# Kernel optimization log

Hardware: AMD Instinct MI355X
Metric: run time of the kernel (lower is better)

The kernel has to match this reference:

```python
import jax, jax.numpy as jnp
import numpy as np

N_EMBD = 768

def setup_inputs() -> dict:
    key = jax.random.key(0)
    k1, k2, k3, k4 = jax.random.split(key, 4)
    B, T, head_size = 16, 1024, 128
    x = jax.random.normal(k1, (B, T, N_EMBD), dtype=jnp.float32)
    # nn.Linear(in, out, bias=False): weight stored as (out, in); we store transposed (in, out)
    s = 1.0 / np.sqrt(N_EMBD)
    Wk = jax.random.uniform(k2, (N_EMBD, head_size), jnp.float32, -s, s)
    Wq = jax.random.uniform(k3, (N_EMBD, head_size), jnp.float32, -s, s)
    Wv = jax.random.uniform(k4, (N_EMBD, head_size), jnp.float32, -s, s)
    return {"x": x, "Wk": Wk, "Wq": Wq, "Wv": Wv}

def reference(x, Wk, Wq, Wv):
    B, T, C = x.shape  # C == n_embd == 768
    k = jnp.einsum('btc,ch->bth', x, Wk)
    q = jnp.einsum('btc,ch->bth', x, Wq)
    v = jnp.einsum('btc,ch->bth', x, Wv)
    # NOTE: original scales by C**-0.5 with C = n_embd (768), not head_size.
    wei = jnp.einsum('bth,bsh->bts', q, k) * (C ** -0.5)  # (B, T, T)
    causal = jnp.tril(jnp.ones((T, T), dtype=bool))
    wei = jnp.where(causal, wei, -jnp.inf)
    wei = jax.nn.softmax(wei, axis=-1)
    # dropout p=0.0 -> identity
    return jnp.einsum('bts,bsh->bth', wei, v)
```

## Files before the change

### kernel.cpp

```cpp
#include <hip/hip_runtime.h>
#include <math.h>

#define NTOK   16384
#define NEMBD  768
#define HDIM   128

typedef __attribute__((ext_vector_type(8)))  short short8;
typedef __attribute__((ext_vector_type(16))) float floatx16;

#define MFMA32(a,b,c) __builtin_amdgcn_mfma_f32_32x32x16_bf16(a,b,c,0,0,0)

__device__ __forceinline__ unsigned short f2bf(float f) {
    unsigned u = __float_as_uint(f);
    u += 0x7fff + ((u >> 16) & 1);
    return (unsigned short)(u >> 16);
}
__device__ __forceinline__ unsigned pack2(float a, float b) {
    return (unsigned)f2bf(a) | ((unsigned)f2bf(b) << 16);
}
__device__ __forceinline__ unsigned pack2_trunc(float a, float b) {
    return __builtin_amdgcn_perm(__float_as_uint(b), __float_as_uint(a),
                                 0x07060302u);
}
__device__ __forceinline__ void gl_lds16(const void* gptr, void* lptr) {
    __builtin_amdgcn_global_load_lds(
        (const __attribute__((address_space(1))) unsigned int*)gptr,
        (__attribute__((address_space(3))) unsigned int*)lptr, 16, 0, 0);
}

__global__ __launch_bounds__(256) void prep_w(
    const float* __restrict__ Wk, const float* __restrict__ Wq,
    const float* __restrict__ Wv, unsigned short* __restrict__ wt)
{
    __shared__ float T[64 * 65];

    const int tid = threadIdx.x;
    const int bw  = blockIdx.x / 24;
    const int rem = blockIdx.x % 24;
    const int ct  = rem >> 1, dh = rem & 1;
    const int c0  = ct * 64, d0 = dh * 64;
    const float* W = (bw == 0) ? Wk : ((bw == 1) ? Wq : Wv);
    const float scale = (bw == 1)
        ? (0.03608439182435161f * 1.4426950408889634f) : 1.0f;

    #pragma unroll
    for (int pass = 0; pass < 4; ++pass) {
        int idx = pass * 256 + tid;
        int c  = idx >> 4;
        int d4 = idx & 15;
        float4 v = ((const float4*)W)[(size_t)(c0 + c) * 32 + dh * 16 + d4];
        v.x *= scale; v.y *= scale; v.z *= scale; v.w *= scale;
        T[(d4 * 4 + 0) * 65 + c] = v.x;
        T[(d4 * 4 + 1) * 65 + c] = v.y;
        T[(d4 * 4 + 2) * 65 + c] = v.z;
        T[(d4 * 4 + 3) * 65 + c] = v.w;
    }
    __syncthreads();

    #pragma unroll
    for (int pass = 0; pass < 2; ++pass) {
        int idx = pass * 256 + tid;
        int d  = idx >> 3;
        int c8 = idx & 7;
        const float* row = &T[d * 65 + c8 * 8];
        uint4 u = make_uint4(pack2(row[0], row[1]), pack2(row[2], row[3]),
                             pack2(row[4], row[5]), pack2(row[6], row[7]));
        *(uint4*)&wt[(size_t)bw * (HDIM * NEMBD) + (size_t)(d0 + d) * NEMBD
                     + c0 + c8 * 8] = u;
    }
}

__global__ __launch_bounds__(256) void qkv_fused(
    const float* __restrict__ x, const unsigned short* __restrict__ wt,
    unsigned short* __restrict__ kb, unsigned short* __restrict__ qb,
    unsigned short* __restrict__ vT)
{
    __shared__ __align__(16) char As[8192];
    __shared__ __align__(16) char Bs[24576];

    const int tid = threadIdx.x, w = tid >> 6, lane = tid & 63;
    const int l31 = lane & 31, h = lane >> 5;
    const int r8 = lane >> 3, c8 = lane & 7;
    const int wm = w >> 1, wn = w & 1;
    const int mtile = blockIdx.x >> 1, nh = blockIdx.x & 1;
    const int m0 = mtile * 64;
    const int nbase = nh * 192;
    const int arow = tid >> 2, ac = tid & 3;

    floatx16 acc[3];
    #pragma unroll
    for (int j = 0; j < 3; ++j)
        #pragma unroll
        for (int i = 0; i < 16; ++i) acc[j][i] = 0.f;

    const float* asrc = x + (size_t)(m0 + arow) * NEMBD + ac * 16;
    float4 a0 = ((const float4*)asrc)[0];
    float4 a1 = ((const float4*)asrc)[1];
    float4 a2 = ((const float4*)asrc)[2];
    float4 a3 = ((const float4*)asrc)[3];

    for (int it = 0; it < 12; ++it) {
        const int k0 = it * 64;
        __syncthreads();
        #pragma unroll
        for (int j = 0; j < 6; ++j) {
            int rowb = w * 48 + j * 8;
            int row  = rowb + r8;
            gl_lds16((const char*)wt + ((size_t)(nbase + row) * NEMBD + k0) * 2
                         + ((c8 ^ (row & 7)) * 16),
                     Bs + rowb * 128);
        }
        {
            uint4 u0 = make_uint4(pack2(a0.x, a0.y), pack2(a0.z, a0.w),
                                  pack2(a1.x, a1.y), pack2(a1.z, a1.w));
            uint4 u1 = make_uint4(pack2(a2.x, a2.y), pack2(a2.z, a2.w),
                                  pack2(a3.x, a3.y), pack2(a3.z, a3.w));
            int cA = 2 * ac, cB = 2 * ac + 1;
            *(uint4*)(As + arow * 128 + ((cA ^ (arow & 7)) * 16)) = u0;
            *(uint4*)(As + arow * 128 + ((cB ^ (arow & 7)) * 16)) = u1;
        }
        if (it < 11) {
            const float4* src = (const float4*)(asrc + (it + 1) * 64);
            a0 = src[0]; a1 = src[1]; a2 = src[2]; a3 = src[3];
        }
        __syncthreads();
        #pragma unroll
        for (int ks = 0; ks < 4; ++ks) {
            int ar = wm * 32 + l31;
            short8 af = *(const short8*)(As + ar * 128
                                         + (((2*ks + h) ^ (ar & 7)) * 16));
            #pragma unroll
            for (int j = 0; j < 3; ++j) {
                int br = wn * 96 + j * 32 + l31;
                short8 bf = *(const short8*)(Bs + br * 128
                                             + (((2*ks + h) ^ (br & 7)) * 16));
                acc[j] = MFMA32(af, bf, acc[j]);
            }
        }
    }

    const int tbase = m0 + wm * 32;
    #pragma unroll
    for (int j = 0; j < 3; ++j) {
        int n0 = nbase + wn * 96 + j * 32;
        if (n0 < 256) {
            unsigned short* outp = (n0 < 128) ? kb : qb;
            int d = (n0 & 127) + l31;
            #pragma unroll
            for (int r = 0; r < 16; ++r) {
                int t = tbase + (r & 3) + 8 * (r >> 2) + 4 * h;
                outp[(size_t)t * HDIM + d] = f2bf(acc[j][r]);
            }
        } else {
            int d = (n0 - 256) + l31, b = m0 >> 10, tloc = (m0 & 1023) + wm * 32;
            #pragma unroll
            for (int g = 0; g < 4; ++g) {
                int t = tloc + 8 * g + 4 * h;
                uint2 u = make_uint2(pack2(acc[j][4*g+0], acc[j][4*g+1]),
                                     pack2(acc[j][4*g+2], acc[j][4*g+3]));
                *(uint2*)((char*)vT + (((size_t)(b * HDIM + d)) * 1024 + t) * 2) = u;
            }
        }
    }
}

__global__ __launch_bounds__(256) void attn_mfma(
    const unsigned short* __restrict__ qb, const unsigned short* __restrict__ kb,
    const unsigned short* __restrict__ vT, float* __restrict__ out)
{
    __shared__ __align__(16) float Obuf[4 * 32 * 128];
    __shared__ float lred[128];

    const int tid = threadIdx.x, w = tid >> 6, lane = tid & 63;
    const int l31 = lane & 31, h = lane >> 5;
    const int u  = blockIdx.x & 255;
    const int b  = u & 15, p = u >> 4;
    const int qt = (blockIdx.x >> 8) ? (31 - p) : p;

    const char* kb_b = (const char*)kb + (size_t)b * (1024 * 256);
    const char* qb_b = (const char*)qb + (size_t)b * (1024 * 256);
    const char* vT_b = (const char*)vT + (size_t)b * (HDIM * 2048);

    short8 qf[8];
    {
        const char* qrow = qb_b + (size_t)(qt * 32 + l31) * 256 + h * 16;
        #pragma unroll
        for (int ks = 0; ks < 8; ++ks)
            qf[ks] = *(const short8*)(qrow + ks * 32);
    }

    floatx16 o[4];
    #pragma unroll
    for (int nt = 0; nt < 4; ++nt)
        #pragma unroll
        for (int i = 0; i < 16; ++i) o[nt][i] = 0.f;
    float l_r = 0.f;

    short8 kf[8];
    if (w <= qt) {
        const char* krow = kb_b + (size_t)(w * 32 + l31) * 256 + h * 16;
        #pragma unroll
        for (int ks = 0; ks < 8; ++ks)
            kf[ks] = *(const short8*)(krow + ks * 32);
    }

    for (int st = w; st <= qt; st += 4) {
        short8 vf[8];
        {
            const char* vrow0 = vT_b + (size_t)l31 * 2048 + (size_t)st * 64 + h * 16;
            #pragma unroll
            for (int nt = 0; nt < 4; ++nt) {
                const char* vr = vrow0 + (size_t)nt * (32 * 2048);
                vf[nt * 2 + 0] = *(const short8*)(vr + 0);
                vf[nt * 2 + 1] = *(const short8*)(vr + 32);
            }
        }
        floatx16 s;
        #pragma unroll
        for (int i = 0; i < 16; ++i) s[i] = 0.f;
        #pragma unroll
        for (int ks = 0; ks < 8; ++ks) s = MFMA32(kf[ks], qf[ks], s);

        if (st + 4 <= qt) {
            const char* krow = kb_b + (size_t)((st + 4) * 32 + l31) * 256 + h * 16;
            #pragma unroll
            for (int ks = 0; ks < 8; ++ks)
                kf[ks] = *(const short8*)(krow + ks * 32);
        }

        if (st == qt) {
            #pragma unroll
            for (int r = 0; r < 16; ++r) {
                int key = (r & 3) + 8 * (r >> 2) + 4 * h;
                if (key > l31) s[r] = -1e30f;
            }
        }
        float p16[16], psum = 0.f;
        #pragma unroll
        for (int r = 0; r < 16; ++r) {
            p16[r] = __builtin_amdgcn_exp2f(s[r]);
            psum += p16[r];
        }
        l_r += psum;

        unsigned own[8], rcv[8];
        #pragma unroll
        for (int i = 0; i < 8; ++i) own[i] = pack2_trunc(p16[2*i], p16[2*i+1]);
        #pragma unroll
        for (int i = 0; i < 8; ++i) rcv[i] = (unsigned)__shfl_xor((int)own[i], 32, 64);
        short8 pf[2];
        {
            union { short8 v; unsigned uu[4]; } f0, f1;
            if (h == 0) {
                f0.uu[0]=own[0]; f0.uu[1]=own[1]; f0.uu[2]=rcv[0]; f0.uu[3]=rcv[1];
                f1.uu[0]=own[4]; f1.uu[1]=own[5]; f1.uu[2]=rcv[4]; f1.uu[3]=rcv[5];
            } else {
                f0.uu[0]=rcv[2]; f0.uu[1]=rcv[3]; f0.uu[2]=own[2]; f0.uu[3]=own[3];
                f1.uu[0]=rcv[6]; f1.uu[1]=rcv[7]; f1.uu[2]=own[6]; f1.uu[3]=own[7];
            }
            pf[0] = f0.v; pf[1] = f1.v;
        }
        #pragma unroll
        for (int nt = 0; nt < 4; ++nt) {
            o[nt] = MFMA32(vf[nt * 2 + 0], pf[0], o[nt]);
            o[nt] = MFMA32(vf[nt * 2 + 1], pf[1], o[nt]);
        }
    }

    l_r += __shfl_xor(l_r, 32, 64);
    if (lane < 32) lred[w * 32 + l31] = l_r;
    {
        float* mybuf = &Obuf[w * 4096];
        #pragma unroll
        for (int nt = 0; nt < 4; ++nt) {
            #pragma unroll
            for (int g = 0; g < 4; ++g) {
                int chunk = nt * 8 + 2 * g + h;
                int slot  = (chunk & 24) | ((chunk & 7) ^ (l31 & 7));
                *((float4*)&mybuf[l31 * 128] + slot) =
                    make_float4(o[nt][4*g+0], o[nt][4*g+1],
                                o[nt][4*g+2], o[nt][4*g+3]);
            }
        }
    }
    __syncthreads();
    {
        int q  = tid >> 3;
        int cb = (tid & 7) * 4;
        float inv = 1.f / (lred[q] + lred[32 + q] + lred[64 + q] + lred[96 + q]);
        #pragma unroll
        for (int cc = 0; cc < 4; ++cc) {
            int chunk = cb + cc;
            int slot  = (chunk & 24) | ((chunk & 7) ^ (q & 7));
            float4 v0 = *((float4*)&Obuf[0 * 4096 + q * 128] + slot);
            float4 v1 = *((float4*)&Obuf[1 * 4096 + q * 128] + slot);
            float4 v2 = *((float4*)&Obuf[2 * 4096 + q * 128] + slot);
            float4 v3 = *((float4*)&Obuf[3 * 4096 + q * 128] + slot);
            float4 v = make_float4((v0.x + v1.x + v2.x + v3.x) * inv,
                                   (v0.y + v1.y + v2.y + v3.y) * inv,
                                   (v0.z + v1.z + v2.z + v3.z) * inv,
                                   (v0.w + v1.w + v2.w + v3.w) * inv);
            *(float4*)&out[((size_t)(b * 1024 + qt * 32 + q)) * HDIM + chunk * 4] = v;
        }
    }
}

extern "C" void kernel_launch(void* const* d_in, const int* in_sizes, int n_in,
                              void* d_out, int out_size, void* d_ws, size_t ws_size,
                              hipStream_t stream)
{
    const float* x  = (const float*)d_in[0];
    const float* Wk = (const float*)d_in[1];
    const float* Wq = (const float*)d_in[2];
    const float* Wv = (const float*)d_in[3];
    float* outp = (float*)d_out;

    char* ws = (char*)d_ws;
    unsigned short* wt = (unsigned short*)(ws);
    unsigned short* kb = (unsigned short*)(ws + 589824);
    unsigned short* qb = (unsigned short*)(ws + 4784128);
    unsigned short* vT = (unsigned short*)(ws + 8978432);

    prep_w<<<72, 256, 0, stream>>>(Wk, Wq, Wv, wt);
    qkv_fused<<<512, 256, 0, stream>>>(x, wt, kb, qb, vT);
    attn_mfma<<<512, 256, 0, stream>>>(qb, kb, vT, outp);
}
```

Baseline: 127.0 us.

## Use hardware bf16 pack, permlane32 swap, block swizzle and MFMA priority hints

Several micro-optimizations land together. The software bf16 rounding is replaced with the v_cvt_pk_bf16_f32 instruction, and the 8 cross-half shuffles in the attention P-fragment exchange are replaced by 4 v_permlane32_swap instructions, removing the h-dependent select. The QKV projection block index is swizzled to change the order tiles are scheduled across CUs. s_setprio is raised around the MFMA chains, and the row-sum accumulation is split into four partial sums for more ILP. Inline asm for permlane32 swap is gfx950-specific, and the swap semantics must match the old shuffle layout.

```diff
diff --git a/kernel.cpp b/kernel.cpp
--- a/kernel.cpp
+++ b/kernel.cpp
@@ -16,7 +16,9 @@
     return (unsigned short)(u >> 16);
 }
 __device__ __forceinline__ unsigned pack2(float a, float b) {
-    return (unsigned)f2bf(a) | ((unsigned)f2bf(b) << 16);
+    unsigned r;
+    asm("v_cvt_pk_bf16_f32 %0, %1, %2" : "=v"(r) : "v"(a), "v"(b));
+    return r;
 }
 __device__ __forceinline__ unsigned pack2_trunc(float a, float b) {
     return __builtin_amdgcn_perm(__float_as_uint(b), __float_as_uint(a),
@@ -82,7 +84,9 @@
     const int l31 = lane & 31, h = lane >> 5;
     const int r8 = lane >> 3, c8 = lane & 7;
     const int wm = w >> 1, wn = w & 1;
-    const int mtile = blockIdx.x >> 1, nh = blockIdx.x & 1;
+    const int bid = blockIdx.x;
+    const int b2  = ((bid & 7) << 6) | (bid >> 3);
+    const int mtile = b2 >> 1, nh = b2 & 1;
     const int m0 = mtile * 64;
     const int nbase = nh * 192;
     const int arow = tid >> 2, ac = tid & 3;
@@ -218,8 +222,10 @@
         floatx16 s;
         #pragma unroll
         for (int i = 0; i < 16; ++i) s[i] = 0.f;
+        __builtin_amdgcn_s_setprio(1);
         #pragma unroll
         for (int ks = 0; ks < 8; ++ks) s = MFMA32(kf[ks], qf[ks], s);
+        __builtin_amdgcn_s_setprio(0);
 
         if (st + 4 <= qt) {
             const char* krow = kb_b + (size_t)((st + 4) * 32 + l31) * 256 + h * 16;
@@ -235,36 +241,40 @@
                 if (key > l31) s[r] = -1e30f;
             }
         }
-        float p16[16], psum = 0.f;
-        #pragma unroll
-        for (int r = 0; r < 16; ++r) {
-            p16[r] = __builtin_amdgcn_exp2f(s[r]);
-            psum += p16[r];
-        }
-        l_r += psum;
-
-        unsigned own[8], rcv[8];
+        float p16[16];
+        float ps0 = 0.f, ps1 = 0.f, ps2 = 0.f, ps3 = 0.f;
+        #pragma unroll
+        for (int r = 0; r < 4; ++r) {
+            p16[4*r+0] = __builtin_amdgcn_exp2f(s[4*r+0]);
+            p16[4*r+1] = __builtin_amdgcn_exp2f(s[4*r+1]);
+            p16[4*r+2] = __builtin_amdgcn_exp2f(s[4*r+2]);
+            p16[4*r+3] = __builtin_amdgcn_exp2f(s[4*r+3]);
+            ps0 += p16[4*r+0]; ps1 += p16[4*r+1];
+            ps2 += p16[4*r+2]; ps3 += p16[4*r+3];
+        }
+        l_r += (ps0 + ps1) + (ps2 + ps3);
+
+        unsigned own[8];
         #pragma unroll
         for (int i = 0; i < 8; ++i) own[i] = pack2_trunc(p16[2*i], p16[2*i+1]);
-        #pragma unroll
-        for (int i = 0; i < 8; ++i) rcv[i] = (unsigned)__shfl_xor((int)own[i], 32, 64);
+        asm("v_permlane32_swap_b32 %0, %1" : "+v"(own[0]), "+v"(own[2]));
+        asm("v_permlane32_swap_b32 %0, %1" : "+v"(own[1]), "+v"(own[3]));
+        asm("v_permlane32_swap_b32 %0, %1" : "+v"(own[4]), "+v"(own[6]));
+        asm("v_permlane32_swap_b32 %0, %1" : "+v"(own[5]), "+v"(own[7]));
         short8 pf[2];
         {
             union { short8 v; unsigned uu[4]; } f0, f1;
-            if (h == 0) {
-                f0.uu[0]=own[0]; f0.uu[1]=own[1]; f0.uu[2]=rcv[0]; f0.uu[3]=rcv[1];
-                f1.uu[0]=own[4]; f1.uu[1]=own[5]; f1.uu[2]=rcv[4]; f1.uu[3]=rcv[5];
-            } else {
-                f0.uu[0]=rcv[2]; f0.uu[1]=rcv[3]; f0.uu[2]=own[2]; f0.uu[3]=own[3];
-                f1.uu[0]=rcv[6]; f1.uu[1]=rcv[7]; f1.uu[2]=own[6]; f1.uu[3]=own[7];
-            }
+            f0.uu[0]=own[0]; f0.uu[1]=own[1]; f0.uu[2]=own[2]; f0.uu[3]=own[3];
+            f1.uu[0]=own[4]; f1.uu[1]=own[5]; f1.uu[2]=own[6]; f1.uu[3]=own[7];
             pf[0] = f0.v; pf[1] = f1.v;
         }
+        __builtin_amdgcn_s_setprio(1);
         #pragma unroll
         for (int nt = 0; nt < 4; ++nt) {
             o[nt] = MFMA32(vf[nt * 2 + 0], pf[0], o[nt]);
             o[nt] = MFMA32(vf[nt * 2 + 1], pf[1], o[nt]);
         }
+        __builtin_amdgcn_s_setprio(0);
     }
 
     l_r += __shfl_xor(l_r, 32, 64);
```

Result: slower. 131.8 us (+3.8%).
